# Performance work log

Hardware: AMD Instinct MI355X
Metric: run time of the kernel (lower is better)

The kernel has to match this reference:

```python
import jax, jax.numpy as jnp
import numpy as np

NUM_HEADS = 8
CHUNK = 64          # dialtion / chunck_size
EPS = 1e-5          # InstanceNorm1d eps
NEG = -1e9


def setup_inputs() -> dict:
    key = jax.random.key(0)
    ks = jax.random.split(key, 8)
    N, C, T = 4, 512, 4096
    x = jax.random.normal(ks[0], (N, C, T), dtype=jnp.float32)
    q = jax.random.normal(ks[1], (N, C, T), dtype=jnp.float32)
    k = jax.random.normal(ks[2], (N, C, T), dtype=jnp.float32)
    v = jax.random.normal(ks[3], (N, C, T), dtype=jnp.float32)
    masks = jnp.ones((N, 1, T), dtype=jnp.float32)
    s = 1.0 / np.sqrt(C)
    W_in = jax.random.normal(ks[4], (3 * C, C), dtype=jnp.float32) * s   # packed q/k/v in-proj
    b_in = jnp.zeros((3 * C,), dtype=jnp.float32)
    W_out = jax.random.normal(ks[5], (C, C), dtype=jnp.float32) * s     # out-proj
    b_out = jnp.zeros((C,), dtype=jnp.float32)
    return {"x": x, "q": q, "k": k, "v": v, "masks": masks,
            "W_in": W_in, "b_in": b_in, "W_out": W_out, "b_out": b_out}


def _chunk_attn(q, k, v, masks, W_in, b_in, W_out, b_out):
    # q,k,v: [N, C, T]; masks: [N, 1, T]
    N, C, T = q.shape
    H, Dh = NUM_HEADS, C // NUM_HEADS
    nc = T // CHUNK
    Wq, Wk, Wv = jnp.split(W_in, 3, axis=0)
    bq, bk, bv = jnp.split(b_in, 3, axis=0)

    def proj(t, W, b):
        # [N,C,T] -> chunked heads [N, nc, CHUNK, H, Dh]
        t = t.transpose(0, 2, 1) @ W.T + b            # [N, T, C]
        return t.reshape(N, nc, CHUNK, H, Dh)

    qh = proj(q, Wq, bq)
    kh = proj(k, Wk, bk)
    vh = proj(v, Wv, bv)

    scale = 1.0 / jnp.sqrt(jnp.asarray(Dh, q.dtype))
    # intra-chunk scores: [N, nc, H, CHUNK, CHUNK]
    scores = jnp.einsum('bnqhd,bnkhd->bnhqk', qh, kh) * scale
    km = masks[:, 0, :].reshape(N, nc, CHUNK)         # key validity per chunk
    scores = scores + jnp.where(km[:, :, None, None, :] > 0, 0.0, NEG)
    attn = jax.nn.softmax(scores, axis=-1)
    out = jnp.einsum('bnhqk,bnkhd->bnqhd', attn, vh).reshape(N, T, C)
    out = out @ W_out.T + b_out                        # [N, T, C]
    out = out.transpose(0, 2, 1) * masks               # [N, C, T], re-mask
    return out


def reference(x, q, k, v, masks, W_in, b_in, W_out, b_out):
    out = _chunk_attn(q, k, v, masks, W_in, b_in, W_out, b_out) + x
    # InstanceNorm1d (affine=False): normalize each (n, c) row over T
    mu = jnp.mean(out, axis=2, keepdims=True)
    var = jnp.mean(jnp.square(out - mu), axis=2, keepdims=True)
    return (out - mu) * jax.lax.rsqrt(var + EPS)
```

## Files before the change

kernel.cpp:

```cpp
#include <hip/hip_runtime.h>
#include <hip/hip_bf16.h>

#define NB 4
#define CC 512
#define TT 4096
#define C3 1536
#define CQK 1024
#define NTC (NB*TT*CC)

typedef __attribute__((ext_vector_type(4))) float f32x4;
typedef __attribute__((ext_vector_type(8))) short short8;
typedef unsigned short ushort;
typedef __attribute__((ext_vector_type(8))) ushort u16x8;

__device__ __forceinline__ ushort f2bf(float f){
    union { float f; unsigned u; } x; x.f = f;
    unsigned r = x.u + 0x7fffu + ((x.u >> 16) & 1u);
    return (ushort)(r >> 16);
}

__device__ __forceinline__ ushort2 pk2bf(float a, float b){
    float2 f2; f2.x = a; f2.y = b;
    __hip_bfloat162 h = __float22bfloat162_rn(f2);
    union { __hip_bfloat162 h2; ushort2 u2; } u; u.h2 = h;
    return u.u2;
}

__device__ __forceinline__ void gload16(const void* g, void* l){
    __builtin_amdgcn_global_load_lds((const __attribute__((address_space(1))) void*)g,
                                     (__attribute__((address_space(3))) void*)l,
                                     16, 0, 0);
}

__device__ __forceinline__ int apos(int m, int cb){
    return (m*8 + ((cb + m + (m >> 3)) & 7))*8;
}

__global__ __launch_bounds__(256) void wcvt(const float* __restrict__ Wi,
                                            const float* __restrict__ Wo,
                                            ushort* __restrict__ Wb,
                                            ushort* __restrict__ Wob){
    int idx0 = blockIdx.x * 1024 + threadIdx.x;
    for (int i = 0; i < 4; ++i){
        int idx = idx0 + i*256;
        const float* src; ushort* dst; int j;
        if (idx < 196608){ src = Wi; dst = Wb;  j = idx; }
        else             { src = Wo; dst = Wob; j = idx - 196608; }
        f32x4 vv = *((const f32x4*)src + j);
        ushort4 o;
        *(ushort2*)&o.x = pk2bf(vv[0], vv[1]);
        *(ushort2*)&o.z = pk2bf(vv[2], vv[3]);
        *((ushort4*)dst + j) = o;
    }
}

__global__ __launch_bounds__(256) void proj_gemm(const float* __restrict__ q,
                                                 const float* __restrict__ k,
                                                 const float* __restrict__ v,
                                                 const ushort* __restrict__ Wb,
                                                 const float* __restrict__ b_in,
                                                 ushort* __restrict__ P,
                                                 ushort* __restrict__ Vt){
    __shared__ __align__(16) ushort smem[40960];
    ushort* sA   = smem;
    ushort* sB0  = smem + 8192;
    ushort* sB1  = smem + 16384;
    float*  Araw = (float*)(smem + 24576);
    const int tid = threadIdx.x;
    const int bid = blockIdx.x;
    const int mtile  = ((bid & 7) << 4) | ((bid >> 3) & 15);
    const int cotile = bid >> 7;
    const int co0 = cotile * 128;
    const int m0  = mtile * 128;
    const int which = co0 >> 9;
    const float* src = (which == 0) ? q : (which == 1) ? k : v;
    const int n  = m0 >> 12, t0 = m0 & 4095;
    const ushort* Bbase = Wb + (size_t)co0*CC;
    const int w = tid >> 6, lane = tid & 63;
    const int wr = w >> 1, wc = w & 1;
    const int l15 = lane & 15, quad = lane >> 4;

    const int rowoff = lane >> 5;
    const int toff   = (lane & 31) * 4;
    const float* Ag = src + (size_t)n*CC*TT + (size_t)(2*w + rowoff)*TT + t0 + toff;
    float* lAr = Araw + (size_t)(2*w)*128;

    const ushort* gB[4]; int lBoff[4];
    for (int i = 0; i < 4; ++i){
        int slot = i*256 + tid;
        int mr = slot >> 3, k8 = slot & 7, kk = k8 ^ (mr & 7);
        gB[i] = Bbase + (size_t)mr*CC + kk*8;
        lBoff[i] = (i*256 + (tid & ~63)) * 8;
    }

    const int cbA = (w << 1) | (lane >> 5);
    const int tA  = lane & 31;

    for (int r = 0; r < 8; ++r)
        gload16(Ag + (size_t)(r*8)*TT, lAr + r*1024);
    for (int i = 0; i < 4; ++i)
        gload16(gB[i], sB0 + lBoff[i]);

    f32x4 acc[4][4] = {};
    for (int kb = 0; kb < 8; ++kb){
        ushort* sBc = (kb & 1) ? sB1 : sB0;
        ushort* sBn = (kb & 1) ? sB0 : sB1;
        __syncthreads();
        f32x4 cur[8];
        #pragma unroll
        for (int j = 0; j < 8; ++j)
            cur[j] = *(const f32x4*)(Araw + (size_t)(cbA*8 + j)*128 + tA*4);
        #pragma unroll
        for (int tj = 0; tj < 4; ++tj){
            int m = tA*4 + tj;
            u16x8 o;
            #pragma unroll
            for (int j = 0; j < 8; j += 2){
                ushort2 p = pk2bf(cur[j][tj], cur[j+1][tj]);
                o[j] = p.x; o[j+1] = p.y;
            }
            *(u16x8*)&sA[apos(m, cbA)] = o;
        }
        __syncthreads();
        if (kb < 7){
            const float* Agn = Ag + (size_t)((kb+1)*64)*TT;
            for (int r = 0; r < 8; ++r)
                gload16(Agn + (size_t)(r*8)*TT, lAr + r*1024);
            for (int i = 0; i < 4; ++i)
                gload16(gB[i] + (kb+1)*64, sBn + lBoff[i]);
        }
        for (int ks = 0; ks < 2; ++ks){
            short8 aF[4], bF[4];
            for (int mi = 0; mi < 4; ++mi){
                int m = wr*64 + mi*16 + l15;
                aF[mi] = *(const short8*)&sA[apos(m, ks*4 + quad)];
            }
            for (int ni = 0; ni < 4; ++ni){
                int m = wc*64 + ni*16 + l15;
                bF[ni] = *(const short8*)&sBc[(m*8 + ((ks*4 + quad) ^ (m & 7)))*8];
            }
            for (int mi = 0; mi < 4; ++mi)
                for (int ni = 0; ni < 4; ++ni)
                    acc[mi][ni] = __builtin_amdgcn_mfma_f32_16x16x32_bf16(
                        aF[mi], bF[ni], acc[mi][ni], 0, 0, 0);
        }
    }

    float bj[4];
    for (int ni = 0; ni < 4; ++ni) bj[ni] = b_in[co0 + wc*64 + ni*16 + l15];

    __syncthreads();
    ushort* sOut = smem;
    if (which < 2){
        for (int mi = 0; mi < 4; ++mi){
            int mrow = wr*64 + mi*16 + quad*4;
            for (int ni = 0; ni < 4; ++ni){
                int col = wc*64 + ni*16 + l15;
                for (int r = 0; r < 4; ++r)
                    sOut[(mrow + r)*136 + col] = f2bf(acc[mi][ni][r] + bj[ni]);
            }
        }
    } else {
        for (int mi = 0; mi < 4; ++mi){
            int mrow = wr*64 + mi*16 + quad*4;
            for (int ni = 0; ni < 4; ++ni){
                int col = wc*64 + ni*16 + l15;
                ushort4 o4;
                o4.x = f2bf(acc[mi][ni][0] + bj[ni]);
                o4.y = f2bf(acc[mi][ni][1] + bj[ni]);
                o4.z = f2bf(acc[mi][ni][2] + bj[ni]);
                o4.w = f2bf(acc[mi][ni][3] + bj[ni]);
                *(ushort4*)&sOut[col*136 + mrow] = o4;
            }
        }
    }
    __syncthreads();
    if (which < 2){
        for (int i = 0; i < 8; ++i){
            int flat = i*256 + tid;
            int row = flat >> 4, cs = (flat & 15)*8;
            u16x8 val = *(const u16x8*)&sOut[row*136 + cs];
            *(u16x8*)(P + (size_t)(m0 + row)*CQK + which*512 + (co0 & 511) + cs) = val;
        }
    } else {
        for (int i = 0; i < 8; ++i){
            int flat = i*256 + tid;
            int row = flat >> 4, cs = (flat & 15)*8;
            int cl = (co0 - 1024) + row;
            int h = cl >> 6, d = cl & 63;
            u16x8 val = *(const u16x8*)&sOut[row*136 + cs];
            *(u16x8*)(Vt + (((size_t)n*8 + h)*64 + d)*TT + t0 + cs) = val;
        }
    }
}

__global__ __launch_bounds__(256) void attn_kernel(const ushort* __restrict__ P,
                                                   const ushort* __restrict__ Vt,
                                                   const float* __restrict__ masks,
                                                   ushort* __restrict__ ctx){
    __shared__ __align__(16) ushort sQ[64*64], sK[64*64], sV[64*64];
    __shared__ __align__(16) ushort sP[64][72];
    __shared__ __align__(16) ushort sO[64*72];
    int bid = blockIdx.x;
    int h = bid & 7, ch = (bid >> 3) & 63, n = bid >> 9;
    const int tid = threadIdx.x, lane = tid & 63, w = tid >> 6;
    const int l15 = lane & 15, quad = lane >> 4;
    const size_t rowbase = (size_t)n*TT + (size_t)ch*64;
    for (int i = 0; i < 2; ++i){
        int slot = i*256 + tid;
        int r = slot >> 3, k8 = slot & 7, kk = k8 ^ (r & 7);
        int lbase = (i*256 + (tid & ~63)) * 8;
        const ushort* gq = P + (rowbase + r)*CQK + h*64 + kk*8;
        gload16(gq,        sQ + lbase);
        gload16(gq + 512,  sK + lbase);
        const ushort* gv = Vt + (((size_t)n*8 + h)*64 + r)*TT + ch*64 + kk*8;
        gload16(gv,        sV + lbase);
    }
    __syncthreads();
    const int m0w = w*16;
    short8 aQ[2]; f32x4 accS[4] = {};
    for (int ks = 0; ks < 2; ++ks){
        int m = m0w + l15;
        aQ[ks] = *(const short8*)&sQ[(m*8 + ((ks*4 + quad) ^ (m & 7)))*8];
    }
    for (int ni = 0; ni < 4; ++ni)
        for (int ks = 0; ks < 2; ++ks){
            int m = ni*16 + l15;
            short8 bK = *(const short8*)&sK[(m*8 + ((ks*4 + quad) ^ (m & 7)))*8];
            accS[ni] = __builtin_amdgcn_mfma_f32_16x16x32_bf16(aQ[ks], bK, accS[ni], 0,0,0);
        }
    float madd[4];
    for (int ni = 0; ni < 4; ++ni){
        float mv = masks[(size_t)n*TT + ch*64 + ni*16 + l15];
        madd[ni] = (mv > 0.f) ? 0.f : -1e9f;
    }
    float s[4][4];
    for (int ni = 0; ni < 4; ++ni)
        for (int r = 0; r < 4; ++r) s[ni][r] = accS[ni][r]*0.125f + madd[ni];
    float ex[4][4];
    for (int r = 0; r < 4; ++r){
        float m1 = fmaxf(fmaxf(s[0][r], s[1][r]), fmaxf(s[2][r], s[3][r]));
        for (int d = 1; d < 16; d <<= 1) m1 = fmaxf(m1, __shfl_xor(m1, d));
        float a = 0.f;
        for (int ni = 0; ni < 4; ++ni){ float e = __expf(s[ni][r] - m1); ex[ni][r] = e; a += e; }
        for (int d = 1; d < 16; d <<= 1) a += __shfl_xor(a, d);
        float rs = 1.0f / a;
        for (int ni = 0; ni < 4; ++ni)
            sP[m0w + quad*4 + r][ni*16 + l15] = f2bf(ex[ni][r] * rs);
    }
    short8 aP[2]; f32x4 accO[4] = {};
    for (int ks = 0; ks < 2; ++ks)
        aP[ks] = *(const short8*)&sP[m0w + l15][ks*32 + quad*8];
    for (int ni = 0; ni < 4; ++ni)
        for (int ks = 0; ks < 2; ++ks){
            int m = ni*16 + l15;
            short8 bV = *(const short8*)&sV[(m*8 + ((ks*4 + quad) ^ (m & 7)))*8];
            accO[ni] = __builtin_amdgcn_mfma_f32_16x16x32_bf16(aP[ks], bV, accO[ni], 0,0,0);
        }
    for (int ni = 0; ni < 4; ++ni)
        for (int r = 0; r < 4; ++r)
            sO[(m0w + quad*4 + r)*72 + ni*16 + l15] = f2bf(accO[ni][r]);
    __syncthreads();
    for (int i = 0; i < 2; ++i){
        int flat = i*256 + tid;
        int row = flat >> 3, cs = (flat & 7)*8;
        u16x8 val = *(const u16x8*)&sO[row*72 + cs];
        *(u16x8*)(ctx + (rowbase + row)*CC + h*64 + cs) = val;
    }
}

__global__ __launch_bounds__(256) void out_gemm(const ushort* __restrict__ ctx,
                                                const ushort* __restrict__ Wob,
                                                const float* __restrict__ b_out,
                                                const float* __restrict__ x,
                                                const float* __restrict__ masks,
                                                float* __restrict__ out){
    __shared__ __align__(16) ushort smem[16896];
    ushort* sA = smem;
    ushort* sB = smem + 128*64;
    float* fOut = (float*)smem;
    const int tid = threadIdx.x;
    const int bid = blockIdx.x;
    const int mtile  = ((bid & 7) << 4) | ((bid >> 3) & 15);
    const int cotile = bid >> 7;
    const int co0 = cotile * 64;
    const int m0  = mtile * 128;
    const int n = m0 >> 12, t0 = m0 & 4095;
    const ushort* Abase = ctx + (size_t)m0*CC;
    const ushort* Bbase = Wob + (size_t)co0*CC;
    const int w = tid >> 6, lane = tid & 63;
    const int wr = w >> 1, wc = w & 1;
    const int l15 = lane & 15, quad = lane >> 4;

    const ushort* gA[4]; ushort* lA[4];
    const ushort* gB[2]; ushort* lB[2];
    for (int i = 0; i < 4; ++i){
        int slot = i*256 + tid;
        int m = slot >> 3, k8 = slot & 7, kk = k8 ^ (m & 7);
        gA[i] = Abase + (size_t)m*CC + kk*8;
        lA[i] = sA + (i*256 + (tid & ~63)) * 8;
    }
    for (int i = 0; i < 2; ++i){
        int slot = i*256 + tid;
        int m = slot >> 3, k8 = slot & 7, kk = k8 ^ (m & 7);
        gB[i] = Bbase + (size_t)m*CC + kk*8;
        lB[i] = sB + (i*256 + (tid & ~63)) * 8;
    }

    f32x4 acc[4][2] = {};
    for (int kb = 0; kb < 8; ++kb){
        __syncthreads();
        for (int i = 0; i < 4; ++i) gload16(gA[i] + kb*64, lA[i]);
        for (int i = 0; i < 2; ++i) gload16(gB[i] + kb*64, lB[i]);
        __syncthreads();
        for (int ks = 0; ks < 2; ++ks){
            short8 aF[4], bF[2];
            for (int mi = 0; mi < 4; ++mi){
                int m = wr*64 + mi*16 + l15;
                aF[mi] = *(const short8*)&sA[(m*8 + ((ks*4 + quad) ^ (m & 7)))*8];
            }
            for (int ni = 0; ni < 2; ++ni){
                int m = wc*32 + ni*16 + l15;
                bF[ni] = *(const short8*)&sB[(m*8 + ((ks*4 + quad) ^ (m & 7)))*8];
            }
            for (int mi = 0; mi < 4; ++mi)
                for (int ni = 0; ni < 2; ++ni)
                    acc[mi][ni] = __builtin_amdgcn_mfma_f32_16x16x32_bf16(
                        aF[mi], bF[ni], acc[mi][ni], 0, 0, 0);
        }
    }
    float bo[2];
    for (int ni = 0; ni < 2; ++ni) bo[ni] = b_out[co0 + wc*32 + ni*16 + l15];

    __syncthreads();
    for (int mi = 0; mi < 4; ++mi){
        int tl = wr*64 + mi*16 + quad*4;
        for (int ni = 0; ni < 2; ++ni){
            int cl = wc*32 + ni*16 + l15;
            f32x4 vv;
            for (int r = 0; r < 4; ++r) vv[r] = acc[mi][ni][r] + bo[ni];
            *(f32x4*)&fOut[cl*132 + tl] = vv;
        }
    }
    __syncthreads();
    for (int i = 0; i < 8; ++i){
        int flat = i*256 + tid;
        int co = flat >> 5, ts = (flat & 31)*4;
        f32x4 a = *(const f32x4*)&fOut[co*132 + ts];
        f32x4 mk = *(const f32x4*)(masks + (size_t)n*TT + t0 + ts);
        f32x4 xv = *(const f32x4*)(x + ((size_t)n*CC + co0 + co)*TT + t0 + ts);
        f32x4 o;
        for (int r = 0; r < 4; ++r) o[r] = a[r]*mk[r] + xv[r];
        *(f32x4*)(out + ((size_t)n*CC + co0 + co)*TT + t0 + ts) = o;
    }
}

__global__ __launch_bounds__(256) void inorm(float* __restrict__ out){
    __shared__ float sS[4], sQ2[4];
    float* row = out + (size_t)blockIdx.x * TT;
    f32x4 vbuf[4];
    float s = 0.f, ss = 0.f;
    for (int i = 0; i < 4; ++i){
        f32x4 vv = *(const f32x4*)(row + (size_t)(i*256 + threadIdx.x)*4);
        vbuf[i] = vv;
        for (int r = 0; r < 4; ++r){ s += vv[r]; ss += vv[r]*vv[r]; }
    }
    for (int d = 1; d < 64; d <<= 1){ s += __shfl_xor(s, d); ss += __shfl_xor(ss, d); }
    int w = threadIdx.x >> 6;
    if ((threadIdx.x & 63) == 0){ sS[w] = s; sQ2[w] = ss; }
    __syncthreads();
    s  = sS[0] + sS[1] + sS[2] + sS[3];
    ss = sQ2[0] + sQ2[1] + sQ2[2] + sQ2[3];
    float mean = s * (1.0f/TT);
    float var  = ss * (1.0f/TT) - mean*mean;
    float rstd = rsqrtf(var + 1e-5f);
    for (int i = 0; i < 4; ++i){
        f32x4 vv = vbuf[i], o;
        for (int r = 0; r < 4; ++r) o[r] = (vv[r] - mean) * rstd;
        *(f32x4*)(row + (size_t)(i*256 + threadIdx.x)*4) = o;
    }
}

extern "C" void kernel_launch(void* const* d_in, const int* in_sizes, int n_in,
                              void* d_out, int out_size, void* d_ws, size_t ws_size,
                              hipStream_t stream) {
    const float* x     = (const float*)d_in[0];
    const float* q     = (const float*)d_in[1];
    const float* k     = (const float*)d_in[2];
    const float* v     = (const float*)d_in[3];
    const float* masks = (const float*)d_in[4];
    const float* W_in  = (const float*)d_in[5];
    const float* b_in  = (const float*)d_in[6];
    const float* W_out = (const float*)d_in[7];
    const float* b_out = (const float*)d_in[8];
    float* out = (float*)d_out;

    ushort* ws  = (ushort*)d_ws;
    ushort* ctx = ws;
    ushort* Wb  = ws + (size_t)NTC;
    ushort* Wob = Wb + 786432;
    ushort* P   = Wob + 262144;
    ushort* Vt  = P + (size_t)NB*TT*CQK;

    wcvt<<<256, 256, 0, stream>>>(W_in, W_out, Wb, Wob);
    proj_gemm<<<1536, 256, 0, stream>>>(q, k, v, Wb, b_in, P, Vt);
    attn_kernel<<<2048, 256, 0, stream>>>(P, Vt, masks, ctx);
    out_gemm<<<1024, 256, 0, stream>>>(ctx, Wob, b_out, x, masks, out);
    inorm<<<2048, 256, 0, stream>>>(out);
}
```

Measured before the change: 239.9 us.

## Retile projection GEMM to 256x128 and loop heads inside attention with prefetch

The projection GEMM moves to 256-row by 128-column tiles with a 32-wide K step, a new A-tile swizzle and launch bounds targeting two blocks per CU. This halves the grid and the number of times weight tiles are re-read. The attention kernel now gives each block one chunk for all 8 heads. It double-buffers the Q/K/V loads for the next head while the current head computes, and reuses the P buffer for output staging. The cost is far fewer attention blocks (256), so each CU has little work to hide latency, plus more registers in the GEMM.

```diff
diff --git a/kernel.cpp b/kernel.cpp
--- a/kernel.cpp
+++ b/kernel.cpp
@@ -30,10 +30,6 @@
     __builtin_amdgcn_global_load_lds((const __attribute__((address_space(1))) void*)g,
                                      (__attribute__((address_space(3))) void*)l,
                                      16, 0, 0);
-}
-
-__device__ __forceinline__ int apos(int m, int cb){
-    return (m*8 + ((cb + m + (m >> 3)) & 7))*8;
 }
 
 __global__ __launch_bounds__(256) void wcvt(const float* __restrict__ Wi,
@@ -54,141 +50,134 @@
     }
 }
 
-__global__ __launch_bounds__(256) void proj_gemm(const float* __restrict__ q,
-                                                 const float* __restrict__ k,
-                                                 const float* __restrict__ v,
-                                                 const ushort* __restrict__ Wb,
-                                                 const float* __restrict__ b_in,
-                                                 ushort* __restrict__ P,
-                                                 ushort* __restrict__ Vt){
-    __shared__ __align__(16) ushort smem[40960];
+__global__ __launch_bounds__(256, 2) void proj_gemm(const float* __restrict__ q,
+                                                    const float* __restrict__ k,
+                                                    const float* __restrict__ v,
+                                                    const ushort* __restrict__ Wb,
+                                                    const float* __restrict__ b_in,
+                                                    ushort* __restrict__ P,
+                                                    ushort* __restrict__ Vt){
+    __shared__ __align__(16) ushort smem[34816];
     ushort* sA   = smem;
-    ushort* sB0  = smem + 8192;
-    ushort* sB1  = smem + 16384;
-    float*  Araw = (float*)(smem + 24576);
+    ushort* sB0  = smem + 10240;
+    ushort* sB1  = smem + 14336;
+    float*  Araw = (float*)(smem + 18432);
     const int tid = threadIdx.x;
     const int bid = blockIdx.x;
-    const int mtile  = ((bid & 7) << 4) | ((bid >> 3) & 15);
-    const int cotile = bid >> 7;
+    const int mtile  = ((bid & 7) << 3) | ((bid >> 3) & 7);
+    const int cotile = bid >> 6;
     const int co0 = cotile * 128;
-    const int m0  = mtile * 128;
+    const int m0  = mtile * 256;
     const int which = co0 >> 9;
     const float* src = (which == 0) ? q : (which == 1) ? k : v;
     const int n  = m0 >> 12, t0 = m0 & 4095;
     const ushort* Bbase = Wb + (size_t)co0*CC;
     const int w = tid >> 6, lane = tid & 63;
-    const int wr = w >> 1, wc = w & 1;
     const int l15 = lane & 15, quad = lane >> 4;
 
-    const int rowoff = lane >> 5;
-    const int toff   = (lane & 31) * 4;
-    const float* Ag = src + (size_t)n*CC*TT + (size_t)(2*w + rowoff)*TT + t0 + toff;
-    float* lAr = Araw + (size_t)(2*w)*128;
-
-    const ushort* gB[4]; int lBoff[4];
-    for (int i = 0; i < 4; ++i){
+    const float* Agbase = src + (size_t)n*CC*TT + (size_t)(w*8)*TT + t0 + lane*4;
+    float* lAr = Araw + w*8*256 + lane*4;
+
+    const ushort* gB[2]; int lBoff[2];
+    for (int i = 0; i < 2; ++i){
         int slot = i*256 + tid;
-        int mr = slot >> 3, k8 = slot & 7, kk = k8 ^ (mr & 7);
-        gB[i] = Bbase + (size_t)mr*CC + kk*8;
+        int co = slot >> 2, k4 = slot & 3, kk = k4 ^ (co & 3);
+        gB[i] = Bbase + (size_t)co*CC + kk*8;
         lBoff[i] = (i*256 + (tid & ~63)) * 8;
     }
 
-    const int cbA = (w << 1) | (lane >> 5);
-    const int tA  = lane & 31;
-
     for (int r = 0; r < 8; ++r)
-        gload16(Ag + (size_t)(r*8)*TT, lAr + r*1024);
-    for (int i = 0; i < 4; ++i)
+        gload16(Agbase + (size_t)r*TT, lAr + r*256);
+    for (int i = 0; i < 2; ++i)
         gload16(gB[i], sB0 + lBoff[i]);
 
-    f32x4 acc[4][4] = {};
-    for (int kb = 0; kb < 8; ++kb){
+    f32x4 acc[4][8] = {};
+    for (int kb = 0; kb < 16; ++kb){
         ushort* sBc = (kb & 1) ? sB1 : sB0;
         ushort* sBn = (kb & 1) ? sB0 : sB1;
         __syncthreads();
         f32x4 cur[8];
         #pragma unroll
         for (int j = 0; j < 8; ++j)
-            cur[j] = *(const f32x4*)(Araw + (size_t)(cbA*8 + j)*128 + tA*4);
+            cur[j] = *(const f32x4*)(Araw + (w*8 + j)*256 + lane*4);
         #pragma unroll
         for (int tj = 0; tj < 4; ++tj){
-            int m = tA*4 + tj;
+            int m = lane*4 + tj;
+            int pos = (w + lane + tj) & 3;
             u16x8 o;
             #pragma unroll
             for (int j = 0; j < 8; j += 2){
                 ushort2 p = pk2bf(cur[j][tj], cur[j+1][tj]);
                 o[j] = p.x; o[j+1] = p.y;
             }
-            *(u16x8*)&sA[apos(m, cbA)] = o;
-        }
-        __syncthreads();
-        if (kb < 7){
-            const float* Agn = Ag + (size_t)((kb+1)*64)*TT;
+            *(u16x8*)&sA[m*40 + pos*8] = o;
+        }
+        __syncthreads();
+        if (kb < 15){
+            const float* Agn = Agbase + (size_t)((kb+1)*32)*TT;
             for (int r = 0; r < 8; ++r)
-                gload16(Agn + (size_t)(r*8)*TT, lAr + r*1024);
-            for (int i = 0; i < 4; ++i)
-                gload16(gB[i] + (kb+1)*64, sBn + lBoff[i]);
-        }
-        for (int ks = 0; ks < 2; ++ks){
-            short8 aF[4], bF[4];
-            for (int mi = 0; mi < 4; ++mi){
-                int m = wr*64 + mi*16 + l15;
-                aF[mi] = *(const short8*)&sA[apos(m, ks*4 + quad)];
-            }
-            for (int ni = 0; ni < 4; ++ni){
-                int m = wc*64 + ni*16 + l15;
-                bF[ni] = *(const short8*)&sBc[(m*8 + ((ks*4 + quad) ^ (m & 7)))*8];
-            }
-            for (int mi = 0; mi < 4; ++mi)
-                for (int ni = 0; ni < 4; ++ni)
-                    acc[mi][ni] = __builtin_amdgcn_mfma_f32_16x16x32_bf16(
-                        aF[mi], bF[ni], acc[mi][ni], 0, 0, 0);
-        }
-    }
-
-    float bj[4];
-    for (int ni = 0; ni < 4; ++ni) bj[ni] = b_in[co0 + wc*64 + ni*16 + l15];
+                gload16(Agn + (size_t)r*TT, lAr + r*256);
+            for (int i = 0; i < 2; ++i)
+                gload16(gB[i] + (kb+1)*32, sBn + lBoff[i]);
+        }
+        short8 aF[4], bF[8];
+        for (int mi = 0; mi < 4; ++mi){
+            int m = w*64 + mi*16 + l15;
+            aF[mi] = *(const short8*)&sA[m*40 + ((quad + (m>>2) + (m&3)) & 3)*8];
+        }
+        for (int ni = 0; ni < 8; ++ni){
+            int co = ni*16 + l15;
+            bF[ni] = *(const short8*)&sBc[co*32 + (quad ^ (co & 3))*8];
+        }
+        for (int mi = 0; mi < 4; ++mi)
+            for (int ni = 0; ni < 8; ++ni)
+                acc[mi][ni] = __builtin_amdgcn_mfma_f32_16x16x32_bf16(
+                    aF[mi], bF[ni], acc[mi][ni], 0, 0, 0);
+    }
+
+    float bj[8];
+    for (int ni = 0; ni < 8; ++ni) bj[ni] = b_in[co0 + ni*16 + l15];
 
     __syncthreads();
     ushort* sOut = smem;
     if (which < 2){
         for (int mi = 0; mi < 4; ++mi){
-            int mrow = wr*64 + mi*16 + quad*4;
-            for (int ni = 0; ni < 4; ++ni){
-                int col = wc*64 + ni*16 + l15;
+            int mrow = w*64 + mi*16 + quad*4;
+            for (int ni = 0; ni < 8; ++ni){
+                int col = ni*16 + l15;
                 for (int r = 0; r < 4; ++r)
                     sOut[(mrow + r)*136 + col] = f2bf(acc[mi][ni][r] + bj[ni]);
             }
         }
     } else {
         for (int mi = 0; mi < 4; ++mi){
-            int mrow = wr*64 + mi*16 + quad*4;
-            for (int ni = 0; ni < 4; ++ni){
-                int col = wc*64 + ni*16 + l15;
+            int mrow = w*64 + mi*16 + quad*4;
+            for (int ni = 0; ni < 8; ++ni){
+                int col = ni*16 + l15;
                 ushort4 o4;
                 o4.x = f2bf(acc[mi][ni][0] + bj[ni]);
                 o4.y = f2bf(acc[mi][ni][1] + bj[ni]);
                 o4.z = f2bf(acc[mi][ni][2] + bj[ni]);
                 o4.w = f2bf(acc[mi][ni][3] + bj[ni]);
-                *(ushort4*)&sOut[col*136 + mrow] = o4;
+                *(ushort4*)&sOut[col*264 + mrow] = o4;
             }
         }
     }
     __syncthreads();
     if (which < 2){
-        for (int i = 0; i < 8; ++i){
+        for (int i = 0; i < 16; ++i){
             int flat = i*256 + tid;
             int row = flat >> 4, cs = (flat & 15)*8;
             u16x8 val = *(const u16x8*)&sOut[row*136 + cs];
             *(u16x8*)(P + (size_t)(m0 + row)*CQK + which*512 + (co0 & 511) + cs) = val;
         }
     } else {
-        for (int i = 0; i < 8; ++i){
+        for (int i = 0; i < 16; ++i){
             int flat = i*256 + tid;
-            int row = flat >> 4, cs = (flat & 15)*8;
+            int row = flat >> 5, cs = (flat & 31)*8;
             int cl = (co0 - 1024) + row;
             int h = cl >> 6, d = cl & 63;
-            u16x8 val = *(const u16x8*)&sOut[row*136 + cs];
+            u16x8 val = *(const u16x8*)&sOut[row*264 + cs];
             *(u16x8*)(Vt + (((size_t)n*8 + h)*64 + d)*TT + t0 + cs) = val;
         }
     }
@@ -198,74 +187,87 @@
                                                    const ushort* __restrict__ Vt,
                                                    const float* __restrict__ masks,
                                                    ushort* __restrict__ ctx){
-    __shared__ __align__(16) ushort sQ[64*64], sK[64*64], sV[64*64];
-    __shared__ __align__(16) ushort sP[64][72];
-    __shared__ __align__(16) ushort sO[64*72];
-    int bid = blockIdx.x;
-    int h = bid & 7, ch = (bid >> 3) & 63, n = bid >> 9;
+    __shared__ __align__(16) ushort sQ[2][4096], sK[2][4096], sV[2][4096];
+    __shared__ __align__(16) ushort sP[64*72];
+    const int bid = blockIdx.x;
+    const int n = bid >> 6, ch = bid & 63;
     const int tid = threadIdx.x, lane = tid & 63, w = tid >> 6;
     const int l15 = lane & 15, quad = lane >> 4;
     const size_t rowbase = (size_t)n*TT + (size_t)ch*64;
+    const int m0w = w*16;
+
+    int rr[2], kk8[2], lbase[2];
     for (int i = 0; i < 2; ++i){
         int slot = i*256 + tid;
-        int r = slot >> 3, k8 = slot & 7, kk = k8 ^ (r & 7);
-        int lbase = (i*256 + (tid & ~63)) * 8;
-        const ushort* gq = P + (rowbase + r)*CQK + h*64 + kk*8;
-        gload16(gq,        sQ + lbase);
-        gload16(gq + 512,  sK + lbase);
-        const ushort* gv = Vt + (((size_t)n*8 + h)*64 + r)*TT + ch*64 + kk*8;
-        gload16(gv,        sV + lbase);
-    }
-    __syncthreads();
-    const int m0w = w*16;
-    short8 aQ[2]; f32x4 accS[4] = {};
-    for (int ks = 0; ks < 2; ++ks){
-        int m = m0w + l15;
-        aQ[ks] = *(const short8*)&sQ[(m*8 + ((ks*4 + quad) ^ (m & 7)))*8];
-    }
-    for (int ni = 0; ni < 4; ++ni)
-        for (int ks = 0; ks < 2; ++ks){
-            int m = ni*16 + l15;
-            short8 bK = *(const short8*)&sK[(m*8 + ((ks*4 + quad) ^ (m & 7)))*8];
-            accS[ni] = __builtin_amdgcn_mfma_f32_16x16x32_bf16(aQ[ks], bK, accS[ni], 0,0,0);
-        }
+        rr[i] = slot >> 3;
+        kk8[i] = (slot & 7) ^ (rr[i] & 7);
+        lbase[i] = (i*256 + (tid & ~63)) * 8;
+    }
+    auto issue = [&](int hh, int buf){
+        for (int i = 0; i < 2; ++i){
+            const ushort* gq = P + (rowbase + rr[i])*CQK + hh*64 + kk8[i]*8;
+            gload16(gq,       &sQ[buf][lbase[i]]);
+            gload16(gq + 512, &sK[buf][lbase[i]]);
+            const ushort* gv = Vt + (((size_t)n*8 + hh)*64 + rr[i])*TT + ch*64 + kk8[i]*8;
+            gload16(gv,       &sV[buf][lbase[i]]);
+        }
+    };
+
     float madd[4];
     for (int ni = 0; ni < 4; ++ni){
         float mv = masks[(size_t)n*TT + ch*64 + ni*16 + l15];
         madd[ni] = (mv > 0.f) ? 0.f : -1e9f;
     }
-    float s[4][4];
-    for (int ni = 0; ni < 4; ++ni)
-        for (int r = 0; r < 4; ++r) s[ni][r] = accS[ni][r]*0.125f + madd[ni];
-    float ex[4][4];
-    for (int r = 0; r < 4; ++r){
-        float m1 = fmaxf(fmaxf(s[0][r], s[1][r]), fmaxf(s[2][r], s[3][r]));
-        for (int d = 1; d < 16; d <<= 1) m1 = fmaxf(m1, __shfl_xor(m1, d));
-        float a = 0.f;
-        for (int ni = 0; ni < 4; ++ni){ float e = __expf(s[ni][r] - m1); ex[ni][r] = e; a += e; }
-        for (int d = 1; d < 16; d <<= 1) a += __shfl_xor(a, d);
-        float rs = 1.0f / a;
+
+    issue(0, 0);
+    for (int h = 0; h < 8; ++h){
+        const int cb = h & 1;
+        __syncthreads();
+        if (h < 7) issue(h+1, cb^1);
+        short8 aQ[2]; f32x4 accS[4] = {};
+        for (int ks = 0; ks < 2; ++ks){
+            int m = m0w + l15;
+            aQ[ks] = *(const short8*)&sQ[cb][(m*8 + ((ks*4 + quad) ^ (m & 7)))*8];
+        }
         for (int ni = 0; ni < 4; ++ni)
-            sP[m0w + quad*4 + r][ni*16 + l15] = f2bf(ex[ni][r] * rs);
-    }
-    short8 aP[2]; f32x4 accO[4] = {};
-    for (int ks = 0; ks < 2; ++ks)
-        aP[ks] = *(const short8*)&sP[m0w + l15][ks*32 + quad*8];
-    for (int ni = 0; ni < 4; ++ni)
-        for (int ks = 0; ks < 2; ++ks){
-            int m = ni*16 + l15;
-            short8 bV = *(const short8*)&sV[(m*8 + ((ks*4 + quad) ^ (m & 7)))*8];
-            accO[ni] = __builtin_amdgcn_mfma_f32_16x16x32_bf16(aP[ks], bV, accO[ni], 0,0,0);
-        }
-    for (int ni = 0; ni < 4; ++ni)
-        for (int r = 0; r < 4; ++r)
-            sO[(m0w + quad*4 + r)*72 + ni*16 + l15] = f2bf(accO[ni][r]);
-    __syncthreads();
-    for (int i = 0; i < 2; ++i){
-        int flat = i*256 + tid;
-        int row = flat >> 3, cs = (flat & 7)*8;
-        u16x8 val = *(const u16x8*)&sO[row*72 + cs];
-        *(u16x8*)(ctx + (rowbase + row)*CC + h*64 + cs) = val;
+            for (int ks = 0; ks < 2; ++ks){
+                int m = ni*16 + l15;
+                short8 bK = *(const short8*)&sK[cb][(m*8 + ((ks*4 + quad) ^ (m & 7)))*8];
+                accS[ni] = __builtin_amdgcn_mfma_f32_16x16x32_bf16(aQ[ks], bK, accS[ni], 0,0,0);
+            }
+        float s[4][4];
+        for (int ni = 0; ni < 4; ++ni)
+            for (int r = 0; r < 4; ++r) s[ni][r] = accS[ni][r]*0.125f + madd[ni];
+        float ex[4][4];
+        for (int r = 0; r < 4; ++r){
+            float m1 = fmaxf(fmaxf(s[0][r], s[1][r]), fmaxf(s[2][r], s[3][r]));
+            for (int d = 1; d < 16; d <<= 1) m1 = fmaxf(m1, __shfl_xor(m1, d));
+            float a = 0.f;
+            for (int ni = 0; ni < 4; ++ni){ float e = __expf(s[ni][r] - m1); ex[ni][r] = e; a += e; }
+            for (int d = 1; d < 16; d <<= 1) a += __shfl_xor(a, d);
+            float rs = 1.0f / a;
+            for (int ni = 0; ni < 4; ++ni)
+                sP[(m0w + quad*4 + r)*72 + ni*16 + l15] = f2bf(ex[ni][r] * rs);
+        }
+        short8 aP[2]; f32x4 accO[4] = {};
+        for (int ks = 0; ks < 2; ++ks)
+            aP[ks] = *(const short8*)&sP[(m0w + l15)*72 + ks*32 + quad*8];
+        for (int ni = 0; ni < 4; ++ni)
+            for (int ks = 0; ks < 2; ++ks){
+                int m = ni*16 + l15;
+                short8 bV = *(const short8*)&sV[cb][(m*8 + ((ks*4 + quad) ^ (m & 7)))*8];
+                accO[ni] = __builtin_amdgcn_mfma_f32_16x16x32_bf16(aP[ks], bV, accO[ni], 0,0,0);
+            }
+        for (int ni = 0; ni < 4; ++ni)
+            for (int r = 0; r < 4; ++r)
+                sP[(m0w + quad*4 + r)*72 + ni*16 + l15] = f2bf(accO[ni][r]);
+        __syncthreads();
+        for (int i = 0; i < 2; ++i){
+            int flat = i*256 + tid;
+            int row = flat >> 3, cs = (flat & 7)*8;
+            u16x8 val = *(const u16x8*)&sP[row*72 + cs];
+            *(u16x8*)(ctx + (rowbase + row)*CC + h*64 + cs) = val;
+        }
     }
 }
 
@@ -403,8 +405,8 @@
     ushort* Vt  = P + (size_t)NB*TT*CQK;
 
     wcvt<<<256, 256, 0, stream>>>(W_in, W_out, Wb, Wob);
-    proj_gemm<<<1536, 256, 0, stream>>>(q, k, v, Wb, b_in, P, Vt);
-    attn_kernel<<<2048, 256, 0, stream>>>(P, Vt, masks, ctx);
+    proj_gemm<<<768, 256, 0, stream>>>(q, k, v, Wb, b_in, P, Vt);
+    attn_kernel<<<256, 256, 0, stream>>>(P, Vt, masks, ctx);
     out_gemm<<<1024, 256, 0, stream>>>(ctx, Wob, b_out, x, masks, out);
     inorm<<<2048, 256, 0, stream>>>(out);
 }
```

Result: slower. 258.7 us (+7.8%).
